# Kernel optimization log

Measured on AMD Instinct MI355X. Metric: run time of the kernel, lower is better.

The kernel has to match this reference:

```python
import jax, jax.numpy as jnp
import numpy as np

H, KD, VD = 8, 64, 64
W = 1.25  # custom weight scale


def layer_norm(x, g, b, eps=1e-5):
    m = x.mean(-1, keepdims=True)
    v = ((x - m) ** 2).mean(-1, keepdims=True)
    return (x - m) * jax.lax.rsqrt(v + eps) * g + b


def cross_attention(x1, x2, wq, wk, wv, wo, bo, wm):
    # Conv1d kernel_size=1 == matmul; channel axis splits as (heads, dim)
    b, s1, _ = x1.shape
    s2 = x2.shape[1]
    q = (x1 @ wq.T).reshape(b, s1, H, KD).transpose(0, 2, 1, 3)  # bhqk
    k = (x2 @ wk.T).reshape(b, s2, H, KD).transpose(0, 2, 1, 3)
    v = (x2 @ wv.T).reshape(b, s2, H, VD).transpose(0, 2, 1, 3)
    attn = jnp.einsum('bhqd,bhsd->bhqs', q, k) * (1.0 / (KD ** 0.5))
    attn = jax.nn.softmax(attn * wm, axis=-1)  # elementwise weight BEFORE softmax
    o = jnp.einsum('bhqs,bhsv->bhqv', attn, v)
    o = o.transpose(0, 2, 1, 3).reshape(b, s1, H * VD)
    return o @ wo.T + bo


def make_wm1(nvars, sl2, patch_num):
    sl = sl2 // 2
    wm = jnp.ones((nvars, sl2), jnp.float32)
    wm = wm.at[:2 * patch_num, :sl].multiply(W)
    wm = wm.at[2 * patch_num:, sl:].multiply(W)
    return wm[None, None]  # broadcast over batch, heads


def make_wm2(nvars, sv, patch_num, patch_num_v):
    wm = jnp.ones((nvars, sv), jnp.float32)
    wm = wm.at[:patch_num, :patch_num_v].multiply(W)
    wm = wm.at[patch_num:2 * patch_num, patch_num_v:2 * patch_num_v].multiply(W)
    wm = wm.at[2 * patch_num:, 2 * patch_num_v:].multiply(W)
    return wm[None, None]


def forward(cords_features, spatial_features, speed_features,
            wq1, wk1, wv1, wo1, bo1, wq2, wk2, wv2, wo2, bo2,
            ln1_g, ln1_b, ln2_g, ln2_b, ln3_g, ln3_b,
            ffn_w1, ffn_b1, ffn_w2, ffn_b2):
    b, nvars, d = cords_features.shape
    patch_num = nvars // 3
    patch_num_v = speed_features.shape[1] // 3
    wm1 = make_wm1(nvars, spatial_features.shape[1], patch_num)
    wm2 = make_wm2(nvars, 3 * patch_num_v, patch_num, patch_num_v)
    x = cross_attention(cords_features, spatial_features, wq1, wk1, wv1, wo1, bo1, wm1)
    x = layer_norm(x + cords_features, ln1_g, ln1_b)
    r2 = x
    x = cross_attention(x, speed_features, wq2, wk2, wv2, wo2, bo2, wm2)
    x = layer_norm(x + r2, ln2_g, ln2_b)
    r3 = x
    h = jax.nn.gelu(x @ ffn_w1.T + ffn_b1, approximate=False)
    x = h @ ffn_w2.T + ffn_b2
    return layer_norm(x + r3, ln3_g, ln3_b)


def setup_inputs():
    key = jax.random.key(0)
    ks = jax.random.split(key, 16)
    D, DF = 512, 2048
    s = 0.02
    inp = {
        'cords_features': jax.random.normal(ks[0], (8, 768, D), jnp.float32),
        'spatial_features': jax.random.normal(ks[1], (8, 1024, D), jnp.float32),
        'speed_features': jax.random.normal(ks[2], (8, 768, D), jnp.float32),
        'wq1': jax.random.normal(ks[3], (H * KD, D)) * s,
        'wk1': jax.random.normal(ks[4], (H * KD, D)) * s,
        'wv1': jax.random.normal(ks[5], (H * VD, D)) * s,
        'wo1': jax.random.normal(ks[6], (D, H * VD)) * s,
        'bo1': jnp.zeros((D,), jnp.float32),
        'wq2': jax.random.normal(ks[7], (H * KD, D)) * s,
        'wk2': jax.random.normal(ks[8], (H * KD, D)) * s,
        'wv2': jax.random.normal(ks[9], (H * VD, D)) * s,
        'wo2': jax.random.normal(ks[10], (D, H * VD)) * s,
        'bo2': jnp.zeros((D,), jnp.float32),
        'ln1_g': jnp.ones((D,), jnp.float32), 'ln1_b': jnp.zeros((D,), jnp.float32),
        'ln2_g': jnp.ones((D,), jnp.float32), 'ln2_b': jnp.zeros((D,), jnp.float32),
        'ln3_g': jnp.ones((D,), jnp.float32), 'ln3_b': jnp.zeros((D,), jnp.float32),
        'ffn_w1': jax.random.normal(ks[11], (DF, D)) * s,
        'ffn_b1': jnp.zeros((DF,), jnp.float32),
        'ffn_w2': jax.random.normal(ks[12], (D, DF)) * s,
        'ffn_b2': jnp.zeros((D,), jnp.float32),
    }
    return inp


def reference(cords_features, spatial_features, speed_features,
              wq1, wk1, wv1, wo1, bo1, wq2, wk2, wv2, wo2, bo2,
              ln1_g, ln1_b, ln2_g, ln2_b, ln3_g, ln3_b,
              ffn_w1, ffn_b1, ffn_w2, ffn_b2):
    return forward(cords_features, spatial_features, speed_features,
                   wq1, wk1, wv1, wo1, bo1, wq2, wk2, wv2, wo2, bo2,
                   ln1_g, ln1_b, ln2_g, ln2_b, ln3_g, ln3_b,
                   ffn_w1, ffn_b1, ffn_w2, ffn_b2)
```

## Files before the change

kernel.cpp:

```cpp
#include <hip/hip_runtime.h>
#include <hip/hip_bf16.h>


#define LN_EPS 1e-5f
#define WSCALE 1.25f

typedef __attribute__((ext_vector_type(8))) short short8;
typedef __attribute__((ext_vector_type(4))) float floatx4;
typedef unsigned short us;

__device__ __forceinline__ float bf2f(us u) {
    union { unsigned int i; float f; } v; v.i = ((unsigned int)u) << 16; return v.f;
}
__device__ __forceinline__ us f2bf(float f) {
    union { float f; unsigned int i; } v; v.f = f;
    return (us)((v.i + 0x7FFFu + ((v.i >> 16) & 1u)) >> 16);
}
__device__ __forceinline__ float gelu_f(float v) {
    float x  = v * 0.70710678118654752f;
    float ax = fabsf(x);
    float t  = 1.0f / (1.0f + 0.3275911f * ax);
    float p  = t * (0.254829592f + t * (-0.284496736f + t * (1.421413741f +
               t * (-1.453152027f + t * 1.061405429f))));
    float er = 1.0f - p * __expf(-ax * ax);
    er = copysignf(er, x);
    return 0.5f * v * (1.0f + er);
}

struct CastArgs {
    const float* src[13];
    us* dst[13];
    int blk_ofs[14];
};
__global__ __launch_bounds__(256) void cast_all(CastArgs a)
{
    int b = blockIdx.x;
    int e = 0;
    while (b >= a.blk_ofs[e + 1]) ++e;
    int i = ((b - a.blk_ofs[e]) * 256 + threadIdx.x) * 8;
    const float* s = a.src[e];
    us* d = a.dst[e];
    float4 x = *(const float4*)(s + i);
    float4 y = *(const float4*)(s + i + 4);
    *(ushort4*)(d + i)     = make_ushort4(f2bf(x.x), f2bf(x.y), f2bf(x.z), f2bf(x.w));
    *(ushort4*)(d + i + 4) = make_ushort4(f2bf(y.x), f2bf(y.y), f2bf(y.z), f2bf(y.w));
}

__global__ __launch_bounds__(256) void gemm64(
    const us* __restrict__ A, const us* __restrict__ Bw,
    const float* __restrict__ bias, us* __restrict__ Cb,
    int M, int N, int K, int flags)
{
    __shared__ us As[64 * 64];
    __shared__ us Bs[64 * 64];

    int t = threadIdx.x;
    int wave = t >> 6, lane = t & 63;
    int m0 = blockIdx.y * 64, n0 = blockIdx.x * 64;
    int wr = (wave >> 1) * 32, wc = (wave & 1) * 32;

    int r_in = lane >> 3;
    int pq   = lane & 7;
    const us* gA[2]; const us* gB[2];
    us* lA[2]; us* lB[2];
#pragma unroll
    for (int c = 0; c < 2; ++c) {
        int r = 16 * wave + 8 * c + r_in;
        int q = pq ^ (r & 7);
        gA[c] = A  + (size_t)(m0 + r) * K + 8 * q;
        gB[c] = Bw + (size_t)(n0 + r) * K + 8 * q;
        lA[c] = As + (16 * wave + 8 * c) * 64;
        lB[c] = Bs + (16 * wave + 8 * c) * 64;
    }

    int fcol = lane & 15, fj = lane >> 4;
    int aoff[2][2], boff[2][2];
#pragma unroll
    for (int mt = 0; mt < 2; ++mt)
#pragma unroll
        for (int kc = 0; kc < 2; ++kc) {
            int fr = wr + 16 * mt + fcol;
            aoff[mt][kc] = fr * 64 + ((kc * 4 + fj) ^ (fr & 7)) * 8;
            int br = wc + 16 * mt + fcol;
            boff[mt][kc] = br * 64 + ((kc * 4 + fj) ^ (br & 7)) * 8;
        }

    floatx4 acc[2][2] = {};

    for (int k0 = 0; k0 < K; k0 += 64) {
        __syncthreads();
#pragma unroll
        for (int c = 0; c < 2; ++c) {
            __builtin_amdgcn_global_load_lds(
                (const __attribute__((address_space(1))) void*)(gA[c] + k0),
                (__attribute__((address_space(3))) void*)lA[c], 16, 0, 0);
            __builtin_amdgcn_global_load_lds(
                (const __attribute__((address_space(1))) void*)(gB[c] + k0),
                (__attribute__((address_space(3))) void*)lB[c], 16, 0, 0);
        }
        __syncthreads();

        short8 af[2][2], bfr[2][2];
#pragma unroll
        for (int mt = 0; mt < 2; ++mt)
#pragma unroll
            for (int kc = 0; kc < 2; ++kc) {
                af[mt][kc]  = *(const short8*)(As + aoff[mt][kc]);
                bfr[mt][kc] = *(const short8*)(Bs + boff[mt][kc]);
            }
#pragma unroll
        for (int kc = 0; kc < 2; ++kc)
#pragma unroll
            for (int mt = 0; mt < 2; ++mt)
#pragma unroll
                for (int nt = 0; nt < 2; ++nt)
                    acc[mt][nt] = __builtin_amdgcn_mfma_f32_16x16x32_bf16(
                        af[mt][kc], bfr[nt][kc], acc[mt][nt], 0, 0, 0);
    }

    int rq = lane >> 4;
#pragma unroll
    for (int mt = 0; mt < 2; ++mt)
#pragma unroll
        for (int nt = 0; nt < 2; ++nt) {
            int col = n0 + wc + 16 * nt + fcol;
            float bv = (flags & 1) ? bias[col] : 0.f;
#pragma unroll
            for (int r = 0; r < 4; ++r) {
                int row = m0 + wr + 16 * mt + rq * 4 + r;
                Cb[(size_t)row * N + col] = f2bf(acc[mt][nt][r] + bv);
            }
        }
}

template<int BM, int BN>
__global__ __launch_bounds__(256) void gemm_t(
    const us* __restrict__ A, const us* __restrict__ Bw,
    const float* __restrict__ bias, float* __restrict__ Cf,
    us* __restrict__ Cb, int M, int N, int K, int flags,
    int vS, us* __restrict__ Vtg)
{
    constexpr int WN = BN / 2;
    constexpr int MT = 4;
    constexpr int NT = WN / 16;
    constexpr int CA = BM / 32;
    constexpr int CB = BN / 32;

    __shared__ us As[BM * 64];
    __shared__ us Bs[BN * 64];

    int t = threadIdx.x;
    int wave = t >> 6, lane = t & 63;
    int m0 = blockIdx.y * BM, n0 = blockIdx.x * BN;
    int wr = (wave >> 1) * 64, wc = (wave & 1) * WN;

    int r_in = lane >> 3;
    int pq   = lane & 7;
    const us* gA[CA]; us* lA[CA];
#pragma unroll
    for (int c = 0; c < CA; ++c) {
        int r = 32 * c + 8 * wave + r_in;
        int q = pq ^ (r & 7);
        gA[c] = A + (size_t)(m0 + r) * K + 8 * q;
        lA[c] = As + (32 * c + 8 * wave) * 64;
    }
    const us* gB[CB]; us* lB[CB];
#pragma unroll
    for (int c = 0; c < CB; ++c) {
        int r = 32 * c + 8 * wave + r_in;
        int q = pq ^ (r & 7);
        gB[c] = Bw + (size_t)(n0 + r) * K + 8 * q;
        lB[c] = Bs + (32 * c + 8 * wave) * 64;
    }

    int fcol = lane & 15, fj = lane >> 4;
    int aoff[MT][2], boff[NT][2];
#pragma unroll
    for (int mt = 0; mt < MT; ++mt)
#pragma unroll
        for (int kc = 0; kc < 2; ++kc) {
            int fr = wr + 16 * mt + fcol;
            aoff[mt][kc] = fr * 64 + ((kc * 4 + fj) ^ (fr & 7)) * 8;
        }
#pragma unroll
    for (int nt = 0; nt < NT; ++nt)
#pragma unroll
        for (int kc = 0; kc < 2; ++kc) {
            int br = wc + 16 * nt + fcol;
            boff[nt][kc] = br * 64 + ((kc * 4 + fj) ^ (br & 7)) * 8;
        }

    floatx4 acc[MT][NT] = {};

    for (int k0 = 0; k0 < K; k0 += 64) {
        __syncthreads();
#pragma unroll
        for (int c = 0; c < CA; ++c)
            __builtin_amdgcn_global_load_lds(
                (const __attribute__((address_space(1))) void*)(gA[c] + k0),
                (__attribute__((address_space(3))) void*)lA[c], 16, 0, 0);
#pragma unroll
        for (int c = 0; c < CB; ++c)
            __builtin_amdgcn_global_load_lds(
                (const __attribute__((address_space(1))) void*)(gB[c] + k0),
                (__attribute__((address_space(3))) void*)lB[c], 16, 0, 0);
        __syncthreads();

        short8 af[MT][2], bfr[NT][2];
#pragma unroll
        for (int mt = 0; mt < MT; ++mt)
#pragma unroll
            for (int kc = 0; kc < 2; ++kc)
                af[mt][kc] = *(const short8*)(As + aoff[mt][kc]);
#pragma unroll
        for (int nt = 0; nt < NT; ++nt)
#pragma unroll
            for (int kc = 0; kc < 2; ++kc)
                bfr[nt][kc] = *(const short8*)(Bs + boff[nt][kc]);
#pragma unroll
        for (int kc = 0; kc < 2; ++kc)
#pragma unroll
            for (int mt = 0; mt < MT; ++mt)
#pragma unroll
                for (int nt = 0; nt < NT; ++nt)
                    acc[mt][nt] = __builtin_amdgcn_mfma_f32_16x16x32_bf16(
                        af[mt][kc], bfr[nt][kc], acc[mt][nt], 0, 0, 0);
    }

    int rq = lane >> 4;
    if (flags & 8) {
        int b = m0 / vS;
        int s_base = m0 - b * vS;
        if (n0 < 512) {
#pragma unroll
            for (int mt = 0; mt < MT; ++mt)
#pragma unroll
                for (int nt = 0; nt < NT; ++nt) {
                    int col = n0 + wc + 16 * nt + fcol;
#pragma unroll
                    for (int r = 0; r < 4; ++r) {
                        int rloc = wr + 16 * mt + rq * 4 + r;
                        Cb[(size_t)(m0 + rloc) * 512 + col] = f2bf(acc[mt][nt][r]);
                    }
                }
        } else {
#pragma unroll
            for (int mt = 0; mt < MT; ++mt)
#pragma unroll
                for (int nt = 0; nt < NT; ++nt) {
                    int cv = n0 + wc + 16 * nt + fcol - 512;
                    int hv = cv >> 6, dv = cv & 63;
                    int sb = s_base + wr + 16 * mt + rq * 4;
                    ushort4 pk = make_ushort4(
                        f2bf(acc[mt][nt][0]), f2bf(acc[mt][nt][1]),
                        f2bf(acc[mt][nt][2]), f2bf(acc[mt][nt][3]));
                    *(ushort4*)(Vtg + ((size_t)(b * 8 + hv) * 64 + dv) * vS + sb) = pk;
                }
        }
        return;
    }

#pragma unroll
    for (int mt = 0; mt < MT; ++mt)
#pragma unroll
        for (int nt = 0; nt < NT; ++nt) {
            int col = n0 + wc + 16 * nt + fcol;
            float bv = (flags & 1) ? bias[col] : 0.f;
#pragma unroll
            for (int r = 0; r < 4; ++r) {
                int row = m0 + wr + 16 * mt + rq * 4 + r;
                float v = acc[mt][nt][r] + bv;
                if (flags & 2) v = gelu_f(v);
                if (flags & 4) Cb[(size_t)row * N + col] = f2bf(v);
                else           Cf[(size_t)row * N + col] = v;
            }
        }
}

__global__ __launch_bounds__(256, 4) void attn_kernel(
    const us* __restrict__ Q, const us* __restrict__ Kf,
    const us* __restrict__ Vg, us* __restrict__ O,
    int S1, int S2, int shift)
{
    __shared__ us Qs[64 * 64];
    __shared__ us Ks[64 * 64];
    __shared__ us Vs[64 * 64];
    __shared__ us Ps[64 * 72];

    int t = threadIdx.x;
    int wave = t >> 6, lane = t & 63;
    int quad = lane >> 4, l15 = lane & 15;
    int q0 = blockIdx.x * 64, hh = blockIdx.y, bb = blockIdx.z;
    int qb = wave * 16;

    int r_in = lane >> 3, pq = lane & 7;
    const us *gK[2], *gV[2];
    us *lK[2], *lV[2];
#pragma unroll
    for (int c2 = 0; c2 < 2; ++c2) {
        int r = qb + 8 * c2 + r_in;
        int lq = pq ^ (r & 7);
        const us* gQ = Q + ((size_t)bb * S1 + q0 + r) * 512 + hh * 64 + 8 * lq;
        gK[c2] = Kf + ((size_t)bb * S2 + r) * 512 + hh * 64 + 8 * lq;
        gV[c2] = Vg + ((size_t)(bb * 8 + hh) * 64 + r) * S2 + 8 * lq;
        us* lQ = Qs + (qb + 8 * c2) * 64;
        lK[c2] = Ks + (qb + 8 * c2) * 64;
        lV[c2] = Vs + (qb + 8 * c2) * 64;
        __builtin_amdgcn_global_load_lds(
            (const __attribute__((address_space(1))) void*)gQ,
            (__attribute__((address_space(3))) void*)lQ, 16, 0, 0);
    }

    int aoffQ[2], poffP[2], boff[4][2];
#pragma unroll
    for (int kc = 0; kc < 2; ++kc) {
        int ph = ((kc * 4 + quad) ^ (l15 & 7)) * 8;
        aoffQ[kc] = (qb + l15) * 64 + ph;
        poffP[kc] = (qb + l15) * 72 + ph;
#pragma unroll
        for (int nt = 0; nt < 4; ++nt)
            boff[nt][kc] = (16 * nt + l15) * 64 + ph;
    }
    int pwoff[4][4];
#pragma unroll
    for (int r = 0; r < 4; ++r) {
        int row = qb + quad * 4 + r;
#pragma unroll
        for (int nt = 0; nt < 4; ++nt) {
            int s = 16 * nt + l15;
            pwoff[nt][r] = row * 72 + (((s >> 3) ^ (row & 7)) * 8) + (s & 7);
        }
    }

    floatx4 acc_o[4] = {};
    float l_part[4] = {0.f, 0.f, 0.f, 0.f};
    int qsh[4];
#pragma unroll
    for (int r = 0; r < 4; ++r) qsh[r] = (q0 + qb + quad * 4 + r) >> shift;

    __syncthreads();
    short8 aq0 = *(const short8*)(Qs + aoffQ[0]);
    short8 aq1 = *(const short8*)(Qs + aoffQ[1]);

    for (int c = 0; c < S2; c += 64) {
        __syncthreads();
#pragma unroll
        for (int c2 = 0; c2 < 2; ++c2) {
            __builtin_amdgcn_global_load_lds(
                (const __attribute__((address_space(1))) void*)(gK[c2] + (size_t)c * 512),
                (__attribute__((address_space(3))) void*)lK[c2], 16, 0, 0);
            __builtin_amdgcn_global_load_lds(
                (const __attribute__((address_space(1))) void*)(gV[c2] + c),
                (__attribute__((address_space(3))) void*)lV[c2], 16, 0, 0);
        }
        __syncthreads();

        floatx4 s_acc[4] = {};
#pragma unroll
        for (int nt = 0; nt < 4; ++nt) {
            short8 bk0 = *(const short8*)(Ks + boff[nt][0]);
            short8 bk1 = *(const short8*)(Ks + boff[nt][1]);
            s_acc[nt] = __builtin_amdgcn_mfma_f32_16x16x32_bf16(aq0, bk0, s_acc[nt], 0, 0, 0);
            s_acc[nt] = __builtin_amdgcn_mfma_f32_16x16x32_bf16(aq1, bk1, s_acc[nt], 0, 0, 0);
        }

#pragma unroll
        for (int nt = 0; nt < 4; ++nt) {
            int srs = (c + 16 * nt + l15) >> shift;
#pragma unroll
            for (int r = 0; r < 4; ++r) {
                float fct = (qsh[r] == srs) ? (0.125f * WSCALE) : 0.125f;
                float p = __expf(s_acc[nt][r] * fct);
                s_acc[nt][r] = p;
                l_part[r] += p;
            }
        }

#pragma unroll
        for (int nt = 0; nt < 4; ++nt)
#pragma unroll
            for (int r = 0; r < 4; ++r)
                Ps[pwoff[nt][r]] = f2bf(s_acc[nt][r]);
        __builtin_amdgcn_wave_barrier();

        short8 ap0 = *(const short8*)(Ps + poffP[0]);
        short8 ap1 = *(const short8*)(Ps + poffP[1]);
#pragma unroll
        for (int nt = 0; nt < 4; ++nt) {
            short8 bv0 = *(const short8*)(Vs + boff[nt][0]);
            short8 bv1 = *(const short8*)(Vs + boff[nt][1]);
            acc_o[nt] = __builtin_amdgcn_mfma_f32_16x16x32_bf16(ap0, bv0, acc_o[nt], 0, 0, 0);
            acc_o[nt] = __builtin_amdgcn_mfma_f32_16x16x32_bf16(ap1, bv1, acc_o[nt], 0, 0, 0);
        }
    }

#pragma unroll
    for (int r = 0; r < 4; ++r) {
#pragma unroll
        for (int off = 8; off; off >>= 1)
            l_part[r] += __shfl_xor(l_part[r], off, 16);
    }
#pragma unroll
    for (int r = 0; r < 4; ++r) {
        float inv = 1.0f / l_part[r];
        size_t base = ((size_t)bb * S1 + q0 + qb + quad * 4 + r) * 512 + hh * 64;
#pragma unroll
        for (int nt = 0; nt < 4; ++nt)
            O[base + 16 * nt + l15] = f2bf(acc_o[nt][r] * inv);
    }
}

__global__ __launch_bounds__(256) void ln_kernel(
    const us* __restrict__ X, const float* __restrict__ R,
    const float* __restrict__ g, const float* __restrict__ bta,
    float* __restrict__ out, us* __restrict__ outb)
{
    int row = blockIdx.x;
    int t   = threadIdx.x;
    const us*    xr = X + (size_t)row * 512;
    const float* rr = R + (size_t)row * 512;
    float v0 = bf2f(xr[t]) + rr[t];
    float v1 = bf2f(xr[t + 256]) + rr[t + 256];
    float s  = v0 + v1;
    float sq = v0 * v0 + v1 * v1;
#pragma unroll
    for (int off = 32; off; off >>= 1) {
        s  += __shfl_xor(s, off, 64);
        sq += __shfl_xor(sq, off, 64);
    }
    __shared__ float ps[4], psq[4];
    int w = t >> 6;
    if ((t & 63) == 0) { ps[w] = s; psq[w] = sq; }
    __syncthreads();
    float S  = ps[0] + ps[1] + ps[2] + ps[3];
    float SQ = psq[0] + psq[1] + psq[2] + psq[3];
    float mean = S * (1.0f / 512.0f);
    float var  = SQ * (1.0f / 512.0f) - mean * mean;
    float inv  = rsqrtf(var + LN_EPS);
    float y0 = (v0 - mean) * inv * g[t] + bta[t];
    float y1 = (v1 - mean) * inv * g[t + 256] + bta[t + 256];
    out[(size_t)row * 512 + t]       = y0;
    out[(size_t)row * 512 + t + 256] = y1;
    if (outb) {
        outb[(size_t)row * 512 + t]       = f2bf(y0);
        outb[(size_t)row * 512 + t + 256] = f2bf(y1);
    }
}

extern "C" void kernel_launch(void* const* d_in, const int* in_sizes, int n_in,
                              void* d_out, int out_size, void* d_ws, size_t ws_size,
                              hipStream_t stream)
{
    const float* cords   = (const float*)d_in[0];
    const float* spatial = (const float*)d_in[1];
    const float* speed   = (const float*)d_in[2];
    const float* wq1 = (const float*)d_in[3];
    const float* wk1 = (const float*)d_in[4];
    const float* wv1 = (const float*)d_in[5];
    const float* wo1 = (const float*)d_in[6];
    const float* bo1 = (const float*)d_in[7];
    const float* wq2 = (const float*)d_in[8];
    const float* wk2 = (const float*)d_in[9];
    const float* wv2 = (const float*)d_in[10];
    const float* wo2 = (const float*)d_in[11];
    const float* bo2 = (const float*)d_in[12];
    const float* ln1g = (const float*)d_in[13];
    const float* ln1b = (const float*)d_in[14];
    const float* ln2g = (const float*)d_in[15];
    const float* ln2b = (const float*)d_in[16];
    const float* ln3g = (const float*)d_in[17];
    const float* ln3b = (const float*)d_in[18];
    const float* fw1 = (const float*)d_in[19];
    const float* fb1 = (const float*)d_in[20];
    const float* fw2 = (const float*)d_in[21];
    const float* fb2 = (const float*)d_in[22];

    const int B = 8, S1 = 768, S2 = 1024, Sv = 768, D = 512, DF = 2048;
    const int M1 = B * S1;
    const int M2 = B * S2;

    char* w = (char*)d_ws;
    us* q_bf = (us*)w;              w += (size_t)M1 * D * 2;
    us* k_bf = (us*)w;              w += (size_t)M2 * D * 2;
    us* vt   = (us*)w;              w += (size_t)M2 * D * 2;
    us* o_bf = (us*)w;              w += (size_t)M1 * D * 2;
    us* p_bf = (us*)w;              w += (size_t)M1 * D * 2;
    float* x1 = (float*)w;          w += (size_t)M1 * D * 4;
    us* cords_bf   = (us*)w;        w += (size_t)M1 * D * 2;
    us* spatial_bf = (us*)w;        w += (size_t)M2 * D * 2;
    us* speed_bf   = (us*)w;        w += (size_t)M1 * D * 2;
    us* wq1b = (us*)w;              w += (size_t)D * D * 2;
    us* wk1b = (us*)w;              w += (size_t)D * D * 2;
    us* wv1b = (us*)w;              w += (size_t)D * D * 2;
    us* wo1b = (us*)w;              w += (size_t)D * D * 2;
    us* wq2b = (us*)w;              w += (size_t)D * D * 2;
    us* wk2b = (us*)w;              w += (size_t)D * D * 2;
    us* wv2b = (us*)w;              w += (size_t)D * D * 2;
    us* wo2b = (us*)w;              w += (size_t)D * D * 2;
    us* fw1b = (us*)w;              w += (size_t)DF * D * 2;
    us* fw2b = (us*)w;              w += (size_t)DF * D * 2;

    us* h_bf  = q_bf;
    us* y_bf  = p_bf;
    us* x1_bf = spatial_bf;
    us* x2_bf = cords_bf;
    float* x2 = (float*)d_out;

    dim3 blk(256);

    {
        CastArgs ca;
        const float* srcs[13] = {cords, spatial, speed, wq1, wk1, wv1, wo1,
                                 wq2, wk2, wv2, wo2, fw1, fw2};
        us* dsts[13] = {cords_bf, spatial_bf, speed_bf, wq1b, wk1b, wv1b, wo1b,
                        wq2b, wk2b, wv2b, wo2b, fw1b, fw2b};
        int ns[13] = {M1 * D, M2 * D, M1 * D, D * D, D * D, D * D, D * D,
                      D * D, D * D, D * D, D * D, DF * D, DF * D};
        int ofs = 0;
        for (int i = 0; i < 13; ++i) {
            ca.src[i] = srcs[i]; ca.dst[i] = dsts[i];
            ca.blk_ofs[i] = ofs; ofs += ns[i] / 2048;
        }
        ca.blk_ofs[13] = ofs;
        cast_all<<<dim3(ofs), blk, 0, stream>>>(ca);
    }

    auto g64  = [](int M, int N) { return dim3(N / 64,  M / 64); };
    auto g128 = [](int M, int N) { return dim3(N / 128, M / 128); };

    gemm64<<<g64(M1, D), blk, 0, stream>>>(cords_bf, wq1b, nullptr, q_bf, M1, D, D, 0);
    gemm_t<128, 128><<<g128(M2, 1024), blk, 0, stream>>>(spatial_bf, wk1b, nullptr, nullptr, k_bf,
                                                         M2, 1024, D, 8, S2, vt);
    attn_kernel<<<dim3(S1 / 64, 8, B), blk, 0, stream>>>(q_bf, k_bf, vt, o_bf, S1, S2, 9);
    gemm64<<<g64(M1, D), blk, 0, stream>>>(o_bf, wo1b, bo1, p_bf, M1, D, D, 1);
    ln_kernel<<<M1, blk, 0, stream>>>(p_bf, cords, ln1g, ln1b, x1, x1_bf);

    gemm64<<<g64(M1, D), blk, 0, stream>>>(x1_bf, wq2b, nullptr, q_bf, M1, D, D, 0);
    gemm_t<128, 128><<<g128(M1, 1024), blk, 0, stream>>>(speed_bf, wk2b, nullptr, nullptr, k_bf,
                                                         M1, 1024, D, 8, Sv, vt);
    attn_kernel<<<dim3(S1 / 64, 8, B), blk, 0, stream>>>(q_bf, k_bf, vt, o_bf, S1, Sv, 8);
    gemm64<<<g64(M1, D), blk, 0, stream>>>(o_bf, wo2b, bo2, p_bf, M1, D, D, 1);
    ln_kernel<<<M1, blk, 0, stream>>>(p_bf, x1, ln2g, ln2b, x2, x2_bf);

    gemm_t<128, 128><<<g128(M1, DF), blk, 0, stream>>>(x2_bf, fw1b, fb1, nullptr, h_bf,
                                                       M1, DF, D, 1 | 2 | 4, 0, nullptr);
    gemm64<<<g64(M1, D), blk, 0, stream>>>(h_bf, fw2b, fb2, y_bf, M1, D, DF, 1);
    ln_kernel<<<M1, blk, 0, stream>>>(y_bf, x2, ln3g, ln3b, (float*)d_out, nullptr);

    (void)in_sizes; (void)n_in; (void)out_size; (void)ws_size;
}
```

Baseline: 367.2 us.

## Double-buffer LDS tiles in GEMM and attention kernels with async prefetch

Converts the GEMM kernels and the attention kernel from single-buffered LDS staging to double buffering. The next K/V or A/B tile is issued with global_load_lds while the current one is consumed, using explicit vmcnt waits and raw s_barrier in place of __syncthreads pairs. This is meant to hide global-load latency behind MFMA work. In exchange LDS use doubles and the attention kernel's launch-bounds occupancy hint drops from 4 to 3, and the hand-counted vmcnt values must match the exact number of outstanding loads.

```diff
diff --git a/kernel.cpp b/kernel.cpp
--- a/kernel.cpp
+++ b/kernel.cpp
@@ -51,8 +51,8 @@
     const float* __restrict__ bias, us* __restrict__ Cb,
     int M, int N, int K, int flags)
 {
-    __shared__ us As[64 * 64];
-    __shared__ us Bs[64 * 64];
+    __shared__ us As[2][64 * 64];
+    __shared__ us Bs[2][64 * 64];
 
     int t = threadIdx.x;
     int wave = t >> 6, lane = t & 63;
@@ -62,15 +62,14 @@
     int r_in = lane >> 3;
     int pq   = lane & 7;
     const us* gA[2]; const us* gB[2];
-    us* lA[2]; us* lB[2];
+    int lofs[2];
 #pragma unroll
     for (int c = 0; c < 2; ++c) {
         int r = 16 * wave + 8 * c + r_in;
         int q = pq ^ (r & 7);
         gA[c] = A  + (size_t)(m0 + r) * K + 8 * q;
         gB[c] = Bw + (size_t)(n0 + r) * K + 8 * q;
-        lA[c] = As + (16 * wave + 8 * c) * 64;
-        lB[c] = Bs + (16 * wave + 8 * c) * 64;
+        lofs[c] = (16 * wave + 8 * c) * 64;
     }
 
     int fcol = lane & 15, fj = lane >> 4;
@@ -87,26 +86,40 @@
 
     floatx4 acc[2][2] = {};
 
-    for (int k0 = 0; k0 < K; k0 += 64) {
-        __syncthreads();
+    auto stage = [&](int buf, int k0) {
 #pragma unroll
         for (int c = 0; c < 2; ++c) {
             __builtin_amdgcn_global_load_lds(
                 (const __attribute__((address_space(1))) void*)(gA[c] + k0),
-                (__attribute__((address_space(3))) void*)lA[c], 16, 0, 0);
+                (__attribute__((address_space(3))) void*)(As[buf] + lofs[c]), 16, 0, 0);
             __builtin_amdgcn_global_load_lds(
                 (const __attribute__((address_space(1))) void*)(gB[c] + k0),
-                (__attribute__((address_space(3))) void*)lB[c], 16, 0, 0);
-        }
-        __syncthreads();
-
+                (__attribute__((address_space(3))) void*)(Bs[buf] + lofs[c]), 16, 0, 0);
+        }
+    };
+
+    int ktrips = K >> 6;
+    stage(0, 0);
+    for (int tt = 0; tt < ktrips; ++tt) {
+        int buf = tt & 1;
+        if (tt + 1 < ktrips) {
+            stage(buf ^ 1, (tt + 1) << 6);
+            asm volatile("s_waitcnt vmcnt(4)" ::: "memory");
+        } else {
+            asm volatile("s_waitcnt vmcnt(0)" ::: "memory");
+        }
+        __builtin_amdgcn_s_barrier();
+        asm volatile("" ::: "memory");
+
+        const us* as_ = As[buf];
+        const us* bs_ = Bs[buf];
         short8 af[2][2], bfr[2][2];
 #pragma unroll
         for (int mt = 0; mt < 2; ++mt)
 #pragma unroll
             for (int kc = 0; kc < 2; ++kc) {
-                af[mt][kc]  = *(const short8*)(As + aoff[mt][kc]);
-                bfr[mt][kc] = *(const short8*)(Bs + boff[mt][kc]);
+                af[mt][kc]  = *(const short8*)(as_ + aoff[mt][kc]);
+                bfr[mt][kc] = *(const short8*)(bs_ + boff[mt][kc]);
             }
 #pragma unroll
         for (int kc = 0; kc < 2; ++kc)
@@ -116,6 +129,9 @@
                 for (int nt = 0; nt < 2; ++nt)
                     acc[mt][nt] = __builtin_amdgcn_mfma_f32_16x16x32_bf16(
                         af[mt][kc], bfr[nt][kc], acc[mt][nt], 0, 0, 0);
+
+        asm volatile("" ::: "memory");
+        __builtin_amdgcn_s_barrier();
     }
 
     int rq = lane >> 4;
@@ -146,8 +162,8 @@
     constexpr int CA = BM / 32;
     constexpr int CB = BN / 32;
 
-    __shared__ us As[BM * 64];
-    __shared__ us Bs[BN * 64];
+    __shared__ us As[2][BM * 64];
+    __shared__ us Bs[2][BN * 64];
 
     int t = threadIdx.x;
     int wave = t >> 6, lane = t & 63;
@@ -156,21 +172,21 @@
 
     int r_in = lane >> 3;
     int pq   = lane & 7;
-    const us* gA[CA]; us* lA[CA];
+    const us* gA[CA]; int lofsA[CA];
 #pragma unroll
     for (int c = 0; c < CA; ++c) {
         int r = 32 * c + 8 * wave + r_in;
         int q = pq ^ (r & 7);
         gA[c] = A + (size_t)(m0 + r) * K + 8 * q;
-        lA[c] = As + (32 * c + 8 * wave) * 64;
-    }
-    const us* gB[CB]; us* lB[CB];
+        lofsA[c] = (32 * c + 8 * wave) * 64;
+    }
+    const us* gB[CB]; int lofsB[CB];
 #pragma unroll
     for (int c = 0; c < CB; ++c) {
         int r = 32 * c + 8 * wave + r_in;
         int q = pq ^ (r & 7);
         gB[c] = Bw + (size_t)(n0 + r) * K + 8 * q;
-        lB[c] = Bs + (32 * c + 8 * wave) * 64;
+        lofsB[c] = (32 * c + 8 * wave) * 64;
     }
 
     int fcol = lane & 15, fj = lane >> 4;
@@ -192,31 +208,45 @@
 
     floatx4 acc[MT][NT] = {};
 
-    for (int k0 = 0; k0 < K; k0 += 64) {
-        __syncthreads();
+    auto stage = [&](int buf, int k0) {
 #pragma unroll
         for (int c = 0; c < CA; ++c)
             __builtin_amdgcn_global_load_lds(
                 (const __attribute__((address_space(1))) void*)(gA[c] + k0),
-                (__attribute__((address_space(3))) void*)lA[c], 16, 0, 0);
+                (__attribute__((address_space(3))) void*)(As[buf] + lofsA[c]), 16, 0, 0);
 #pragma unroll
         for (int c = 0; c < CB; ++c)
             __builtin_amdgcn_global_load_lds(
                 (const __attribute__((address_space(1))) void*)(gB[c] + k0),
-                (__attribute__((address_space(3))) void*)lB[c], 16, 0, 0);
-        __syncthreads();
-
+                (__attribute__((address_space(3))) void*)(Bs[buf] + lofsB[c]), 16, 0, 0);
+    };
+
+    int ktrips = K >> 6;
+    stage(0, 0);
+    for (int tt = 0; tt < ktrips; ++tt) {
+        int buf = tt & 1;
+        if (tt + 1 < ktrips) {
+            stage(buf ^ 1, (tt + 1) << 6);
+            asm volatile("s_waitcnt vmcnt(8)" ::: "memory");
+        } else {
+            asm volatile("s_waitcnt vmcnt(0)" ::: "memory");
+        }
+        __builtin_amdgcn_s_barrier();
+        asm volatile("" ::: "memory");
+
+        const us* as_ = As[buf];
+        const us* bs_ = Bs[buf];
         short8 af[MT][2], bfr[NT][2];
 #pragma unroll
         for (int mt = 0; mt < MT; ++mt)
 #pragma unroll
             for (int kc = 0; kc < 2; ++kc)
-                af[mt][kc] = *(const short8*)(As + aoff[mt][kc]);
+                af[mt][kc] = *(const short8*)(as_ + aoff[mt][kc]);
 #pragma unroll
         for (int nt = 0; nt < NT; ++nt)
 #pragma unroll
             for (int kc = 0; kc < 2; ++kc)
-                bfr[nt][kc] = *(const short8*)(Bs + boff[nt][kc]);
+                bfr[nt][kc] = *(const short8*)(bs_ + boff[nt][kc]);
 #pragma unroll
         for (int kc = 0; kc < 2; ++kc)
 #pragma unroll
@@ -225,6 +255,9 @@
                 for (int nt = 0; nt < NT; ++nt)
                     acc[mt][nt] = __builtin_amdgcn_mfma_f32_16x16x32_bf16(
                         af[mt][kc], bfr[nt][kc], acc[mt][nt], 0, 0, 0);
+
+        asm volatile("" ::: "memory");
+        __builtin_amdgcn_s_barrier();
     }
 
     int rq = lane >> 4;
@@ -277,14 +310,14 @@
         }
 }
 
-__global__ __launch_bounds__(256, 4) void attn_kernel(
+__global__ __launch_bounds__(256, 3) void attn_kernel(
     const us* __restrict__ Q, const us* __restrict__ Kf,
     const us* __restrict__ Vg, us* __restrict__ O,
     int S1, int S2, int shift)
 {
     __shared__ us Qs[64 * 64];
-    __shared__ us Ks[64 * 64];
-    __shared__ us Vs[64 * 64];
+    __shared__ us Ks[2][64 * 64];
+    __shared__ us Vs[2][64 * 64];
     __shared__ us Ps[64 * 72];
 
     int t = threadIdx.x;
@@ -295,7 +328,7 @@
 
     int r_in = lane >> 3, pq = lane & 7;
     const us *gK[2], *gV[2];
-    us *lK[2], *lV[2];
+    int lofs[2];
 #pragma unroll
     for (int c2 = 0; c2 < 2; ++c2) {
         int r = qb + 8 * c2 + r_in;
@@ -303,12 +336,10 @@
         const us* gQ = Q + ((size_t)bb * S1 + q0 + r) * 512 + hh * 64 + 8 * lq;
         gK[c2] = Kf + ((size_t)bb * S2 + r) * 512 + hh * 64 + 8 * lq;
         gV[c2] = Vg + ((size_t)(bb * 8 + hh) * 64 + r) * S2 + 8 * lq;
-        us* lQ = Qs + (qb + 8 * c2) * 64;
-        lK[c2] = Ks + (qb + 8 * c2) * 64;
-        lV[c2] = Vs + (qb + 8 * c2) * 64;
+        lofs[c2] = (qb + 8 * c2) * 64;
         __builtin_amdgcn_global_load_lds(
             (const __attribute__((address_space(1))) void*)gQ,
-            (__attribute__((address_space(3))) void*)lQ, 16, 0, 0);
+            (__attribute__((address_space(3))) void*)(Qs + lofs[c2]), 16, 0, 0);
     }
 
     int aoffQ[2], poffP[2], boff[4][2];
@@ -338,35 +369,53 @@
 #pragma unroll
     for (int r = 0; r < 4; ++r) qsh[r] = (q0 + qb + quad * 4 + r) >> shift;
 
-    __syncthreads();
+    auto stageKV = [&](int buf, int cc) {
+#pragma unroll
+        for (int c2 = 0; c2 < 2; ++c2) {
+            __builtin_amdgcn_global_load_lds(
+                (const __attribute__((address_space(1))) void*)(gK[c2] + (size_t)cc * 512),
+                (__attribute__((address_space(3))) void*)(Ks[buf] + lofs[c2]), 16, 0, 0);
+            __builtin_amdgcn_global_load_lds(
+                (const __attribute__((address_space(1))) void*)(gV[c2] + cc),
+                (__attribute__((address_space(3))) void*)(Vs[buf] + lofs[c2]), 16, 0, 0);
+        }
+    };
+
+    stageKV(0, 0);
+    asm volatile("s_waitcnt vmcnt(4)" ::: "memory");
+    __builtin_amdgcn_s_barrier();
+    asm volatile("" ::: "memory");
     short8 aq0 = *(const short8*)(Qs + aoffQ[0]);
     short8 aq1 = *(const short8*)(Qs + aoffQ[1]);
 
-    for (int c = 0; c < S2; c += 64) {
-        __syncthreads();
-#pragma unroll
-        for (int c2 = 0; c2 < 2; ++c2) {
-            __builtin_amdgcn_global_load_lds(
-                (const __attribute__((address_space(1))) void*)(gK[c2] + (size_t)c * 512),
-                (__attribute__((address_space(3))) void*)lK[c2], 16, 0, 0);
-            __builtin_amdgcn_global_load_lds(
-                (const __attribute__((address_space(1))) void*)(gV[c2] + c),
-                (__attribute__((address_space(3))) void*)lV[c2], 16, 0, 0);
-        }
-        __syncthreads();
+    int ntile = S2 >> 6;
+    for (int ti = 0; ti < ntile; ++ti) {
+        int buf = ti & 1;
+        if (ti + 1 < ntile) {
+            stageKV(buf ^ 1, (ti + 1) << 6);
+            asm volatile("s_waitcnt vmcnt(4)" ::: "memory");
+        } else {
+            asm volatile("s_waitcnt vmcnt(0)" ::: "memory");
+        }
+        __builtin_amdgcn_s_barrier();
+        asm volatile("" ::: "memory");
+
+        const us* ks_ = Ks[buf];
+        const us* vs_ = Vs[buf];
+        int cbase = ti << 6;
 
         floatx4 s_acc[4] = {};
 #pragma unroll
         for (int nt = 0; nt < 4; ++nt) {
-            short8 bk0 = *(const short8*)(Ks + boff[nt][0]);
-            short8 bk1 = *(const short8*)(Ks + boff[nt][1]);
+            short8 bk0 = *(const short8*)(ks_ + boff[nt][0]);
+            short8 bk1 = *(const short8*)(ks_ + boff[nt][1]);
             s_acc[nt] = __builtin_amdgcn_mfma_f32_16x16x32_bf16(aq0, bk0, s_acc[nt], 0, 0, 0);
             s_acc[nt] = __builtin_amdgcn_mfma_f32_16x16x32_bf16(aq1, bk1, s_acc[nt], 0, 0, 0);
         }
 
 #pragma unroll
         for (int nt = 0; nt < 4; ++nt) {
-            int srs = (c + 16 * nt + l15) >> shift;
+            int srs = (cbase + 16 * nt + l15) >> shift;
 #pragma unroll
             for (int r = 0; r < 4; ++r) {
                 float fct = (qsh[r] == srs) ? (0.125f * WSCALE) : 0.125f;
@@ -387,11 +436,14 @@
         short8 ap1 = *(const short8*)(Ps + poffP[1]);
 #pragma unroll
         for (int nt = 0; nt < 4; ++nt) {
-            short8 bv0 = *(const short8*)(Vs + boff[nt][0]);
-            short8 bv1 = *(const short8*)(Vs + boff[nt][1]);
+            short8 bv0 = *(const short8*)(vs_ + boff[nt][0]);
+            short8 bv1 = *(const short8*)(vs_ + boff[nt][1]);
             acc_o[nt] = __builtin_amdgcn_mfma_f32_16x16x32_bf16(ap0, bv0, acc_o[nt], 0, 0, 0);
             acc_o[nt] = __builtin_amdgcn_mfma_f32_16x16x32_bf16(ap1, bv1, acc_o[nt], 0, 0, 0);
         }
+
+        asm volatile("" ::: "memory");
+        __builtin_amdgcn_s_barrier();
     }
 
 #pragma unroll
```

Result: faster. 357.3 us (-2.7%).
